# Kernel tuning notes

Measured on AMD Instinct MI355X. Metric: run time of the kernel, lower is better.

Reference implementation:

```python
import jax, jax.numpy as jnp
import numpy as np


def setup_inputs() -> dict:
    key = jax.random.key(0)
    k1, k2 = jax.random.split(key)
    N, P, SMK, L = 256, 64, 2048, 32
    inp = jax.random.normal(k1, (N, P, SMK, 2), dtype=jnp.float32)
    # channel taps; in the original these are randn scaled by sqrt(power/2)
    cof = jax.random.normal(k2, (N, P, L, 2), dtype=jnp.float32) * 0.1
    return {"input": inp, "cof": cof, "M": 64}


def reference(input, cof, M):
    # input: (N, P, SMK, 2) real/imag stacked; cof: (N, P, L, 2)
    N, P, SMK, _ = input.shape
    L = cof.shape[2]
    sig = (input[..., 0] + 1j * input[..., 1]).reshape(N * P, SMK)   # complex64
    h = (cof[..., 0] + 1j * cof[..., 1]).reshape(N * P, L)
    # torch path: conv1d with time-reversed taps and padding=L-1 == FULL linear
    # convolution; four real convs == one complex conv.
    out_c = jax.vmap(lambda s, k: jnp.convolve(s, k, mode="full"))(sig, h)  # (N*P, SMK+L-1)
    output = jnp.stack([out_c.real, out_c.imag], axis=-1).reshape(N, P, SMK + L - 1, 2)
    # H_t = FFT of zero-padded taps along the tap axis (length M)
    cof_zp = jnp.pad(cof, ((0, 0), (0, 0), (0, M - L), (0, 0)))
    Hc = jnp.fft.fft(cof_zp[..., 0] + 1j * cof_zp[..., 1], axis=-1)  # (N, P, M)
    H_t = jnp.stack([Hc.real, Hc.imag], axis=-1)                      # (N, P, M, 2)
    return output, H_t
```

## Files before the change

kernel.cpp:

```cpp
#include <hip/hip_runtime.h>
#include <math.h>

#define SMK    2048
#define TAPS   32
#define OUTLEN (SMK + TAPS - 1)
#define PAD    32
#define SLOTS  (PAD + SMK + PAD)
#define MDFT   64

typedef float v2f __attribute__((ext_vector_type(2)));

__device__ __forceinline__ int swz(int p) { return p ^ ((p >> 4) & 15); }

__device__ __forceinline__ float rfl(float x) {
    return __int_as_float(__builtin_amdgcn_readfirstlane(__float_as_int(x)));
}

__global__ __launch_bounds__(256)
__attribute__((amdgpu_waves_per_eu(4, 4)))
void conv_kernel(const float* __restrict__ input,
                 const float* __restrict__ cof,
                 float* __restrict__ out0,
                 float* __restrict__ out1)
{
    __shared__ float2 s_sig[SLOTS];
    __shared__ float2 s_tw[MDFT];

    const int tid = threadIdx.x;
    const int row = blockIdx.x;

    const float4* gin = (const float4*)(input + (size_t)row * (SMK * 2));
    #pragma unroll
    for (int k = 0; k < 4; ++k) {
        float4 v = gin[tid + 256 * k];
        int i0 = PAD + 2 * (tid + 256 * k);
        s_sig[swz(i0)]     = make_float2(v.x, v.y);
        s_sig[swz(i0 + 1)] = make_float2(v.z, v.w);
    }
    if (tid < PAD) {
        s_sig[swz(tid)] = make_float2(0.f, 0.f);
    } else if (tid < 2 * PAD) {
        s_sig[swz(SMK + tid)] = make_float2(0.f, 0.f);
    }
    if (tid >= 64 && tid < 128) {
        int j = tid - 64;
        float sv, cv;
        __sincosf(-2.0f * (float)M_PI * (float)j / (float)MDFT, &sv, &cv);
        s_tw[j] = make_float2(cv, sv);
    }

    const float2* __restrict__ ct = (const float2*)(cof + (size_t)row * (TAPS * 2));
    float hre[TAPS], him[TAPS];
    #pragma unroll
    for (int l = 0; l < TAPS; ++l) {
        float2 tv = ct[l];
        hre[l] = rfl(tv.x);
        him[l] = rfl(tv.y);
    }
    __syncthreads();

    const int t0 = tid * 8;

    float2 win[39];
    #pragma unroll
    for (int m = 0; m < 39; ++m) win[m] = s_sig[swz(t0 + 1 + m)];

    v2f accA[8], accB[8];
    #pragma unroll
    for (int k = 0; k < 8; ++k) { accA[k] = (v2f)(0.f); accB[k] = (v2f)(0.f); }

    #pragma unroll
    for (int l = 0; l < TAPS; ++l) {
        const v2f hv = { hre[l], him[l] };
        #pragma unroll
        for (int k = 0; k < 8; ++k) {
            const float2 s = win[k + 31 - l];
            accA[k] = __builtin_elementwise_fma((v2f){ s.x, s.x }, hv, accA[k]);
            accB[k] = __builtin_elementwise_fma((v2f){ s.y, s.y }, hv, accB[k]);
        }
    }

    float2* go2 = (float2*)(out0 + (size_t)row * (OUTLEN * 2));
    #pragma unroll
    for (int k = 0; k < 8; ++k)
        go2[t0 + k] = make_float2(accA[k].x - accB[k].y, accA[k].y + accB[k].x);

    if (tid < MDFT) {
        const int kk = tid;
        v2f aA = (v2f)(0.f), aB = (v2f)(0.f);
        #pragma unroll
        for (int l = 0; l < TAPS; ++l) {
            const v2f hv = { hre[l], him[l] };
            float2 w = s_tw[(kk * l) & (MDFT - 1)];
            aA = __builtin_elementwise_fma((v2f){ w.x, w.x }, hv, aA);
            aB = __builtin_elementwise_fma((v2f){ w.y, w.y }, hv, aB);
        }
        ((float2*)out1)[(size_t)row * MDFT + kk] =
            make_float2(aA.x - aB.y, aA.y + aB.x);
    }
    else if (tid >= 128 && tid < 128 + (OUTLEN - SMK)) {
        const int t = SMK + (tid - 128);
        v2f aA = (v2f)(0.f), aB = (v2f)(0.f);
        #pragma unroll
        for (int l = 0; l < TAPS; ++l) {
            const v2f hv = { hre[l], him[l] };
            float2 s = s_sig[swz(PAD + t - l)];
            aA = __builtin_elementwise_fma((v2f){ s.x, s.x }, hv, aA);
            aB = __builtin_elementwise_fma((v2f){ s.y, s.y }, hv, aB);
        }
        go2[t] = make_float2(aA.x - aB.y, aA.y + aB.x);
    }
}

extern "C" void kernel_launch(void* const* d_in, const int* in_sizes, int n_in,
                              void* d_out, int out_size, void* d_ws, size_t ws_size,
                              hipStream_t stream)
{
    const float* input = (const float*)d_in[0];
    const float* cof   = (const float*)d_in[1];

    const int NP = in_sizes[0] / (SMK * 2);

    float* out0 = (float*)d_out;
    float* out1 = out0 + (size_t)NP * OUTLEN * 2;

    conv_kernel<<<NP, 256, 0, stream>>>(input, cof, out0, out1);
}
```

Baseline: 146.4 us.

## Make blocks persistent over several rows and prefetch the next row into registers

The launch drops from one block per row to a fixed grid of 2048 blocks, each handling 8 rows strided by the grid size. Each block prefetches the next row's signal and taps into registers while it computes the current row, so global load latency overlaps with the FMA work. The occupancy hint is lowered from 4 to 3 waves per EU to leave room for the staging registers. Grid size and rows per block are hardcoded, so correctness depends on NP being exactly 16384, and the extra barriers plus lower occupancy may offset the gain.

```diff
diff --git a/kernel.cpp b/kernel.cpp
--- a/kernel.cpp
+++ b/kernel.cpp
@@ -7,6 +7,8 @@
 #define PAD    32
 #define SLOTS  (PAD + SMK + PAD)
 #define MDFT   64
+#define ROWS_PER_BLOCK 8
+#define NBLOCKS 2048
 
 typedef float v2f __attribute__((ext_vector_type(2)));
 
@@ -17,7 +19,7 @@
 }
 
 __global__ __launch_bounds__(256)
-__attribute__((amdgpu_waves_per_eu(4, 4)))
+__attribute__((amdgpu_waves_per_eu(3, 3)))
 void conv_kernel(const float* __restrict__ input,
                  const float* __restrict__ cof,
                  float* __restrict__ out0,
@@ -27,16 +29,7 @@
     __shared__ float2 s_tw[MDFT];
 
     const int tid = threadIdx.x;
-    const int row = blockIdx.x;
 
-    const float4* gin = (const float4*)(input + (size_t)row * (SMK * 2));
-    #pragma unroll
-    for (int k = 0; k < 4; ++k) {
-        float4 v = gin[tid + 256 * k];
-        int i0 = PAD + 2 * (tid + 256 * k);
-        s_sig[swz(i0)]     = make_float2(v.x, v.y);
-        s_sig[swz(i0 + 1)] = make_float2(v.z, v.w);
-    }
     if (tid < PAD) {
         s_sig[swz(tid)] = make_float2(0.f, 0.f);
     } else if (tid < 2 * PAD) {
@@ -49,66 +42,109 @@
         s_tw[j] = make_float2(cv, sv);
     }
 
-    const float2* __restrict__ ct = (const float2*)(cof + (size_t)row * (TAPS * 2));
-    float hre[TAPS], him[TAPS];
-    #pragma unroll
-    for (int l = 0; l < TAPS; ++l) {
-        float2 tv = ct[l];
-        hre[l] = rfl(tv.x);
-        him[l] = rfl(tv.y);
-    }
-    __syncthreads();
-
-    const int t0 = tid * 8;
-
-    float2 win[39];
-    #pragma unroll
-    for (int m = 0; m < 39; ++m) win[m] = s_sig[swz(t0 + 1 + m)];
-
-    v2f accA[8], accB[8];
-    #pragma unroll
-    for (int k = 0; k < 8; ++k) { accA[k] = (v2f)(0.f); accB[k] = (v2f)(0.f); }
-
-    #pragma unroll
-    for (int l = 0; l < TAPS; ++l) {
-        const v2f hv = { hre[l], him[l] };
+    float4 stg[4];
+    float  hre[TAPS], him[TAPS];
+    {
+        const float4* g = (const float4*)(input + (size_t)blockIdx.x * (SMK * 2));
         #pragma unroll
-        for (int k = 0; k < 8; ++k) {
-            const float2 s = win[k + 31 - l];
-            accA[k] = __builtin_elementwise_fma((v2f){ s.x, s.x }, hv, accA[k]);
-            accB[k] = __builtin_elementwise_fma((v2f){ s.y, s.y }, hv, accB[k]);
+        for (int k = 0; k < 4; ++k) stg[k] = g[tid + 256 * k];
+        const float2* ct = (const float2*)(cof + (size_t)blockIdx.x * (TAPS * 2));
+        #pragma unroll
+        for (int l = 0; l < TAPS; ++l) {
+            float2 tv = ct[l];
+            hre[l] = rfl(tv.x);
+            him[l] = rfl(tv.y);
         }
     }
 
-    float2* go2 = (float2*)(out0 + (size_t)row * (OUTLEN * 2));
-    #pragma unroll
-    for (int k = 0; k < 8; ++k)
-        go2[t0 + k] = make_float2(accA[k].x - accB[k].y, accA[k].y + accB[k].x);
+    #pragma unroll 1
+    for (int it = 0; it < ROWS_PER_BLOCK; ++it) {
+        const size_t r = (size_t)blockIdx.x + (size_t)NBLOCKS * it;
 
-    if (tid < MDFT) {
-        const int kk = tid;
-        v2f aA = (v2f)(0.f), aB = (v2f)(0.f);
+        __syncthreads();
+        #pragma unroll
+        for (int k = 0; k < 4; ++k) {
+            int i0 = PAD + 2 * (tid + 256 * k);
+            s_sig[swz(i0)]     = make_float2(stg[k].x, stg[k].y);
+            s_sig[swz(i0 + 1)] = make_float2(stg[k].z, stg[k].w);
+        }
+        __syncthreads();
+
+        float4 nstg[4];
+        float  nhre[TAPS], nhim[TAPS];
+        const bool more = (it + 1 < ROWS_PER_BLOCK);
+        if (more) {
+            const float4* gn = (const float4*)(input + (r + NBLOCKS) * (size_t)(SMK * 2));
+            #pragma unroll
+            for (int k = 0; k < 4; ++k) nstg[k] = gn[tid + 256 * k];
+            const float2* ctn = (const float2*)(cof + (r + NBLOCKS) * (size_t)(TAPS * 2));
+            #pragma unroll
+            for (int l = 0; l < TAPS; ++l) {
+                float2 tv = ctn[l];
+                nhre[l] = tv.x;
+                nhim[l] = tv.y;
+            }
+        }
+
+        const int t0 = tid * 8;
+        float2 win[39];
+        #pragma unroll
+        for (int m = 0; m < 39; ++m) win[m] = s_sig[swz(t0 + 1 + m)];
+
+        v2f accA[8], accB[8];
+        #pragma unroll
+        for (int k = 0; k < 8; ++k) { accA[k] = (v2f)(0.f); accB[k] = (v2f)(0.f); }
+
         #pragma unroll
         for (int l = 0; l < TAPS; ++l) {
             const v2f hv = { hre[l], him[l] };
-            float2 w = s_tw[(kk * l) & (MDFT - 1)];
-            aA = __builtin_elementwise_fma((v2f){ w.x, w.x }, hv, aA);
-            aB = __builtin_elementwise_fma((v2f){ w.y, w.y }, hv, aB);
+            #pragma unroll
+            for (int k = 0; k < 8; ++k) {
+                const float2 s = win[k + 31 - l];
+                accA[k] = __builtin_elementwise_fma((v2f){ s.x, s.x }, hv, accA[k]);
+                accB[k] = __builtin_elementwise_fma((v2f){ s.y, s.y }, hv, accB[k]);
+            }
         }
-        ((float2*)out1)[(size_t)row * MDFT + kk] =
-            make_float2(aA.x - aB.y, aA.y + aB.x);
-    }
-    else if (tid >= 128 && tid < 128 + (OUTLEN - SMK)) {
-        const int t = SMK + (tid - 128);
-        v2f aA = (v2f)(0.f), aB = (v2f)(0.f);
+
+        float2* go2 = (float2*)(out0 + r * (size_t)(OUTLEN * 2));
         #pragma unroll
-        for (int l = 0; l < TAPS; ++l) {
-            const v2f hv = { hre[l], him[l] };
-            float2 s = s_sig[swz(PAD + t - l)];
-            aA = __builtin_elementwise_fma((v2f){ s.x, s.x }, hv, aA);
-            aB = __builtin_elementwise_fma((v2f){ s.y, s.y }, hv, aB);
+        for (int k = 0; k < 8; ++k)
+            go2[t0 + k] = make_float2(accA[k].x - accB[k].y, accA[k].y + accB[k].x);
+
+        if (tid < MDFT) {
+            const int kk = tid;
+            v2f aA = (v2f)(0.f), aB = (v2f)(0.f);
+            #pragma unroll
+            for (int l = 0; l < TAPS; ++l) {
+                const v2f hv = { hre[l], him[l] };
+                float2 w = s_tw[(kk * l) & (MDFT - 1)];
+                aA = __builtin_elementwise_fma((v2f){ w.x, w.x }, hv, aA);
+                aB = __builtin_elementwise_fma((v2f){ w.y, w.y }, hv, aB);
+            }
+            ((float2*)out1)[r * MDFT + kk] = make_float2(aA.x - aB.y, aA.y + aB.x);
         }
-        go2[t] = make_float2(aA.x - aB.y, aA.y + aB.x);
+        else if (tid >= 128 && tid < 128 + (OUTLEN - SMK)) {
+            const int t = SMK + (tid - 128);
+            v2f aA = (v2f)(0.f), aB = (v2f)(0.f);
+            #pragma unroll
+            for (int l = 0; l < TAPS; ++l) {
+                const v2f hv = { hre[l], him[l] };
+                float2 s = s_sig[swz(PAD + t - l)];
+                aA = __builtin_elementwise_fma((v2f){ s.x, s.x }, hv, aA);
+                aB = __builtin_elementwise_fma((v2f){ s.y, s.y }, hv, aB);
+            }
+            go2[t] = make_float2(aA.x - aB.y, aA.y + aB.x);
+        }
+
+        if (more) {
+            #pragma unroll
+            for (int k = 0; k < 4; ++k) stg[k] = nstg[k];
+            #pragma unroll
+            for (int l = 0; l < TAPS; ++l) {
+                hre[l] = rfl(nhre[l]);
+                him[l] = rfl(nhim[l]);
+            }
+        }
     }
 }
 
@@ -124,5 +160,5 @@
     float* out0 = (float*)d_out;
     float* out1 = out0 + (size_t)NP * OUTLEN * 2;
 
-    conv_kernel<<<NP, 256, 0, stream>>>(input, cof, out0, out1);
+    conv_kernel<<<NBLOCKS, 256, 0, stream>>>(input, cof, out0, out1);
 }
```

New measurement: 534.7 us. 265% more time.

## Restructure conv to 2-output chunks with 16B-aligned stores and higher occupancy

Applied to the files above, without the earlier changes.

Replaces the per-thread 8-output register window with a loop over four 2-output chunks, each reading small 9-element LDS windows per 8-tap group. This cuts register pressure so occupancy can rise, with launch bounds requesting 8 blocks per CU. Output indices are offset by row parity so each pair of complex outputs can be written as one aligned float4 store. The leftover edge outputs are remapped per parity to cover what the chunks miss. The cost is more LDS reads and less register reuse per FMA.

```diff
diff --git a/kernel.cpp b/kernel.cpp
--- a/kernel.cpp
+++ b/kernel.cpp
@@ -16,8 +16,7 @@
     return __int_as_float(__builtin_amdgcn_readfirstlane(__float_as_int(x)));
 }
 
-__global__ __launch_bounds__(256)
-__attribute__((amdgpu_waves_per_eu(4, 4)))
+__global__ __launch_bounds__(256, 8)
 void conv_kernel(const float* __restrict__ input,
                  const float* __restrict__ cof,
                  float* __restrict__ out0,
@@ -28,6 +27,7 @@
 
     const int tid = threadIdx.x;
     const int row = blockIdx.x;
+    const int S   = 1 - (row & 1);
 
     const float4* gin = (const float4*)(input + (size_t)row * (SMK * 2));
     #pragma unroll
@@ -59,31 +59,41 @@
     }
     __syncthreads();
 
-    const int t0 = tid * 8;
+    float2* go2 = (float2*)(out0 + (size_t)row * (OUTLEN * 2));
 
-    float2 win[39];
-    #pragma unroll
-    for (int m = 0; m < 39; ++m) win[m] = s_sig[swz(t0 + 1 + m)];
+    #pragma unroll 1
+    for (int j = 0; j < 4; ++j) {
+        const int t0 = 2 * tid + 1 + S + 512 * j;
 
-    v2f accA[8], accB[8];
-    #pragma unroll
-    for (int k = 0; k < 8; ++k) { accA[k] = (v2f)(0.f); accB[k] = (v2f)(0.f); }
+        v2f accA[2], accB[2];
+        #pragma unroll
+        for (int k = 0; k < 2; ++k) { accA[k] = (v2f)(0.f); accB[k] = (v2f)(0.f); }
 
-    #pragma unroll
-    for (int l = 0; l < TAPS; ++l) {
-        const v2f hv = { hre[l], him[l] };
         #pragma unroll
-        for (int k = 0; k < 8; ++k) {
-            const float2 s = win[k + 31 - l];
-            accA[k] = __builtin_elementwise_fma((v2f){ s.x, s.x }, hv, accA[k]);
-            accB[k] = __builtin_elementwise_fma((v2f){ s.y, s.y }, hv, accB[k]);
+        for (int c = 0; c < 4; ++c) {
+            const int base = PAD + t0 - 8 * c - 7;
+            float2 w2[9];
+            #pragma unroll
+            for (int i = 0; i < 9; ++i) w2[i] = s_sig[swz(base + i)];
+
+            #pragma unroll
+            for (int lp = 0; lp < 8; ++lp) {
+                const int l = 8 * c + lp;
+                const v2f hv = { hre[l], him[l] };
+                #pragma unroll
+                for (int k = 0; k < 2; ++k) {
+                    const float2 s = w2[k - lp + 7];
+                    accA[k] = __builtin_elementwise_fma((v2f){ s.x, s.x }, hv, accA[k]);
+                    accB[k] = __builtin_elementwise_fma((v2f){ s.y, s.y }, hv, accB[k]);
+                }
+            }
+            __builtin_amdgcn_sched_barrier(0);
         }
+
+        float4* p4 = (float4*)__builtin_assume_aligned((void*)&go2[t0], 16);
+        *p4 = make_float4(accA[0].x - accB[0].y, accA[0].y + accB[0].x,
+                          accA[1].x - accB[1].y, accA[1].y + accB[1].x);
     }
-
-    float2* go2 = (float2*)(out0 + (size_t)row * (OUTLEN * 2));
-    #pragma unroll
-    for (int k = 0; k < 8; ++k)
-        go2[t0 + k] = make_float2(accA[k].x - accB[k].y, accA[k].y + accB[k].x);
 
     if (tid < MDFT) {
         const int kk = tid;
@@ -98,8 +108,11 @@
         ((float2*)out1)[(size_t)row * MDFT + kk] =
             make_float2(aA.x - aB.y, aA.y + aB.x);
     }
-    else if (tid >= 128 && tid < 128 + (OUTLEN - SMK)) {
-        const int t = SMK + (tid - 128);
+    else if (tid >= 128 && tid <= 158) {
+        const int idx = tid - 128;
+        int t;
+        if (S == 0) t = (idx < 30) ? (2049 + idx) : 0;
+        else        t = (idx < 29) ? (2050 + idx) : (idx == 29 ? 1 : 0);
         v2f aA = (v2f)(0.f), aB = (v2f)(0.f);
         #pragma unroll
         for (int l = 0; l < TAPS; ++l) {
```

Result: slower. 185.0 us (+26.4%).
